# Kernel tuning notes

Measured on AMD Instinct MI355X. Metric: run time of the kernel, lower is better.

The kernel has to match this reference:

```python
import jax, jax.numpy as jnp
import numpy as np

HIDDEN = 256   # HIDDEN_NUM
INPUT = 4      # fixed input_size
B, T = 128, 512


def _lstm_dir(xs, wi, wh, bi, bh):
    """Single-direction LSTM scan. xs: [T,B,D]; wi: [4H,D]; wh: [4H,H]; bi,bh: [4H].
    PyTorch gate order: i, f, g, o. Returns hidden states [T,B,H]."""
    Tn, Bn, _ = xs.shape
    Hn = wh.shape[1]
    # precompute input contribution for all timesteps (tiny D -> one big GEMM)
    gx = jnp.einsum('tbd,gd->tbg', xs, wi) + bi + bh  # [T,B,4H]

    def step(carry, g):
        h, c = carry
        g = g + h @ wh.T
        i, f, gg, o = jnp.split(g, 4, axis=-1)
        c = jax.nn.sigmoid(f) * c + jax.nn.sigmoid(i) * jnp.tanh(gg)
        h = jax.nn.sigmoid(o) * jnp.tanh(c)
        return (h, c), h

    init = (jnp.zeros((Bn, Hn), xs.dtype), jnp.zeros((Bn, Hn), xs.dtype))
    _, hs = jax.lax.scan(step, init, gx)
    return hs


def _lstm_bidir(xs, w_ih, w_hh, b_ih, b_hh):
    """xs: [T,B,D]; weights stacked over direction: w_ih [2,4H,D] etc. -> [T,B,2H]."""
    fwd = _lstm_dir(xs, w_ih[0], w_hh[0], b_ih[0], b_hh[0])
    bwd = _lstm_dir(xs[::-1], w_ih[1], w_hh[1], b_ih[1], b_hh[1])[::-1]
    return jnp.concatenate([fwd, bwd], axis=-1)


def setup_inputs() -> dict:
    key = jax.random.key(0)
    ks = jax.random.split(key, 12)
    k = 1.0 / np.sqrt(HIDDEN)
    u = lambda kk, shape: jax.random.uniform(kk, shape, jnp.float32, -k, k)
    H4 = 4 * HIDDEN
    return {
        'x': jax.random.normal(ks[0], (B, T, INPUT), jnp.float32),
        # layer 0 (input size 4), stacked [fwd, bwd]
        'w_ih0': u(ks[1], (2, H4, INPUT)),
        'w_hh0': u(ks[2], (2, H4, HIDDEN)),
        'b_ih0': u(ks[3], (2, H4)),
        'b_hh0': u(ks[4], (2, H4)),
        # layer 1 (input size 2H from bidirectional layer 0)
        'w_ih1': u(ks[5], (2, H4, 2 * HIDDEN)),
        'w_hh1': u(ks[6], (2, H4, HIDDEN)),
        'b_ih1': u(ks[7], (2, H4)),
        'b_hh1': u(ks[8], (2, H4)),
        # final linear: HIDDEN*2 -> 2
        'fc_w': u(ks[9], (2, 2 * HIDDEN)),
        'fc_b': u(ks[10], (2,)),
    }


def reference(x, w_ih0, w_hh0, b_ih0, b_hh0, w_ih1, w_hh1, b_ih1, b_hh1, fc_w, fc_b):
    xs = jnp.transpose(x, (1, 0, 2))                 # [T,B,4] (seq-major like torch)
    h0 = _lstm_bidir(xs, w_ih0, w_hh0, b_ih0, b_hh0)  # [T,B,2H]
    h1 = _lstm_bidir(h0, w_ih1, w_hh1, b_ih1, b_hh1)  # [T,B,2H]
    pooled = jnp.mean(h1, axis=0)                     # [B,2H]
    return pooled @ fc_w.T + fc_b                     # [B,2]
```

## Files before the change

kernel.cpp:

```cpp
#include <hip/hip_runtime.h>
#include <hip/hip_bf16.h>


typedef __bf16 bf16;
typedef __bf16 bf16x8 __attribute__((ext_vector_type(8)));
typedef float  f32x4  __attribute__((ext_vector_type(4)));
typedef unsigned int u32;
typedef unsigned long long u64;
typedef u64 u64x2 __attribute__((ext_vector_type(2)));

#define T_SEQ 512
#define BATCH 128
#define HID   256

#define H0_BYTES   67239936ULL
#define H1_BYTES   262144ULL
#define POOL_BYTES 262144ULL
#define FL0_OFF    (H0_BYTES + H1_BYTES + POOL_BYTES)
#define FL1_OFF    (FL0_OFF + 4096ULL)

#define MFMA16(a, b, c) __builtin_amdgcn_mfma_f32_16x16x32_bf16((a), (b), (c), 0, 0, 0)
#define AL(p)     __hip_atomic_load((p), __ATOMIC_RELAXED, __HIP_MEMORY_SCOPE_AGENT)
#define AS(p, v)  __hip_atomic_store((p), (v), __ATOMIC_RELAXED, __HIP_MEMORY_SCOPE_AGENT)

__device__ __forceinline__ float fsig(float v) {
    return __builtin_amdgcn_rcpf(1.0f + __expf(-v));
}
__device__ __forceinline__ float ftanh(float v) {
    float a = fabsf(v);
    float e = __expf(-2.0f * a);
    float r = (1.0f - e) * __builtin_amdgcn_rcpf(1.0f + e);
    return v < 0.0f ? -r : r;
}

__global__ void k_init(unsigned int* ws_u, int* flags0, int* flags1) {
    const int t = blockIdx.x * 256 + threadIdx.x;
    ws_u[t] = 0u;
    ws_u[(size_t)513 * 16384 + t] = 0u;
    unsigned int* h1u = ws_u + (H0_BYTES / 4);
    h1u[t] = 0u;
    h1u[32768 + t] = 0u;
    if (t < 1024) flags0[t] = 0;
    if (t < 2048) flags1[t] = 0;
}

__global__ __launch_bounds__(256, 1) void k_l0(
    const float* __restrict__ x, const float* __restrict__ wih,
    const float* __restrict__ whh, const float* __restrict__ bih,
    const float* __restrict__ bhh, bf16* __restrict__ h0,
    int* __restrict__ flags)
{
    __shared__ __align__(16) bf16 Hs[64][20];

    const int blk = blockIdx.x;
    const int dir = blk >> 5, bh = (blk >> 4) & 1, g = blk & 15;
    const int tid = threadIdx.x, wave = tid >> 6, lane = tid & 63;
    const int l15 = lane & 15, q = lane >> 4;
    const int j = g * 16 + l15;

    bf16x8 Bf[4][8];
#pragma unroll
    for (int tg = 0; tg < 4; ++tg) {
        const float* wr = whh + ((size_t)(dir * 1024 + tg * 256 + j)) * 256 + q * 8;
#pragma unroll
        for (int kt = 0; kt < 8; ++kt) {
            f32x4 aa = *(const f32x4*)(wr + kt * 32);
            f32x4 bb = *(const f32x4*)(wr + kt * 32 + 4);
            bf16x8 f;
            f[0] = (bf16)aa[0]; f[1] = (bf16)aa[1]; f[2] = (bf16)aa[2]; f[3] = (bf16)aa[3];
            f[4] = (bf16)bb[0]; f[5] = (bf16)bb[1]; f[6] = (bf16)bb[2]; f[7] = (bf16)bb[3];
            Bf[tg][kt] = f;
        }
    }
    float biasg[4], wx[4][4];
#pragma unroll
    for (int tg = 0; tg < 4; ++tg) {
        const int n = dir * 1024 + tg * 256 + j;
        biasg[tg] = bih[n] + bhh[n];
#pragma unroll
        for (int d2 = 0; d2 < 4; ++d2) wx[tg][d2] = wih[(size_t)n * 4 + d2];
    }

    float c4[4] = {0.f, 0.f, 0.f, 0.f};
    const int arow  = bh * 64 + wave * 16 + l15;
    const int lrow0 = wave * 16 + q * 4;
    const int mrow0 = bh * 64 + lrow0;
    const int srow = tid >> 2, scg = (tid & 3) * 4;
    int* fgrp = flags + (dir * 2 + bh) * 256;
    int budget = 30000000;

#pragma unroll 1
    for (int s = 1; s <= T_SEQ; ++s) {
        const int t_in = dir ? (T_SEQ - s) : (s - 1);

        f32x4 xv[4];
#pragma unroll
        for (int r = 0; r < 4; ++r)
            xv[r] = *(const f32x4*)(x + ((size_t)(mrow0 + r) * T_SEQ + t_in) * 4);
        f32x4 acc[4];
#pragma unroll
        for (int tg = 0; tg < 4; ++tg) {
#pragma unroll
            for (int r = 0; r < 4; ++r) {
                acc[tg][r] = biasg[tg] + xv[r][0] * wx[tg][0] + xv[r][1] * wx[tg][1]
                                       + xv[r][2] * wx[tg][2] + xv[r][3] * wx[tg][3];
            }
        }

        if (lane < 16) {
            const int need = s - 1;
            while (AL(fgrp + lane * 16) < need) {
                if (--budget < 0) break;
            }
        }
        asm volatile("" ::: "memory");

        const u64* hsrc = (const u64*)(h0 + ((size_t)(dir * 513 + (s - 1)) * BATCH + arow) * HID)
                          + q * 2;
        u64 av[16];
#pragma unroll
        for (int kt = 0; kt < 8; ++kt) {
            av[2 * kt]     = AL(hsrc + kt * 8);
            av[2 * kt + 1] = AL(hsrc + kt * 8 + 1);
        }
#pragma unroll
        for (int kt = 0; kt < 8; ++kt) {
            u64x2 t2; t2[0] = av[2 * kt]; t2[1] = av[2 * kt + 1];
            const bf16x8 A = __builtin_bit_cast(bf16x8, t2);
            acc[0] = MFMA16(A, Bf[0][kt], acc[0]);
            acc[1] = MFMA16(A, Bf[1][kt], acc[1]);
            acc[2] = MFMA16(A, Bf[2][kt], acc[2]);
            acc[3] = MFMA16(A, Bf[3][kt], acc[3]);
        }

#pragma unroll
        for (int r = 0; r < 4; ++r) {
            const float iv = fsig(acc[0][r]);
            const float fv = fsig(acc[1][r]);
            const float gv = ftanh(acc[2][r]);
            const float ov = fsig(acc[3][r]);
            c4[r] = fv * c4[r] + iv * gv;
            const float hv = ov * ftanh(c4[r]);
            Hs[lrow0 + r][l15] = (bf16)hv;
        }
        __syncthreads();
        {
            const u64 hv8 = *(const u64*)&Hs[srow][scg];
            u64* dst = (u64*)(h0 + ((size_t)(dir * 513 + s) * BATCH + bh * 64 + srow) * HID
                              + g * 16 + scg);
            AS(dst, hv8);
        }
        __syncthreads();
        if (tid == 0) AS(fgrp + g * 16, s);
    }
}

__global__ __launch_bounds__(256, 1) void k_l1(
    const float* __restrict__ wih1, const float* __restrict__ whh1,
    const float* __restrict__ bih1, const float* __restrict__ bhh1,
    bf16* __restrict__ h0, bf16* __restrict__ h1,
    float* __restrict__ pooled, int* __restrict__ flags)
{
    __shared__ float Gs[4][32][17];
    __shared__ __align__(16) bf16 Hs[32][20];
    __shared__ __align__(16) bf16 As1[32][264];

    const int blk = blockIdx.x;
    const int dir = blk >> 6, bq = (blk >> 4) & 3, g = blk & 15;
    const int tid = threadIdx.x, wave = tid >> 6, lane = tid & 63;
    const int l15 = lane & 15, q = lane >> 4;
    const int n = dir * 1024 + wave * 256 + g * 16 + l15;

    bf16x8 Bf[24];
#pragma unroll
    for (int kt = 0; kt < 24; ++kt) {
        const int k = kt * 32 + q * 8;
        const float* src = (kt < 8) ? (whh1 + (size_t)n * 256 + k)
                                    : (wih1 + (size_t)n * 512 + (k - 256));
        f32x4 aa = *(const f32x4*)src;
        f32x4 bb = *(const f32x4*)(src + 4);
        bf16x8 f;
        f[0] = (bf16)aa[0]; f[1] = (bf16)aa[1]; f[2] = (bf16)aa[2]; f[3] = (bf16)aa[3];
        f[4] = (bf16)bb[0]; f[5] = (bf16)bb[1]; f[6] = (bf16)bb[2]; f[7] = (bf16)bb[3];
        Bf[kt] = f;
    }
    const float biasw = bih1[n] + bhh1[n];
    const int r0 = tid >> 4, colu = tid & 15;
    float cst[2] = {0.f, 0.f}, pool[2] = {0.f, 0.f};
    int* fgrp = flags + (dir * 4 + bq) * 256;
    int budget = 30000000;

#pragma unroll 1
    for (int s = 1; s <= T_SEQ; ++s) {
        const int slotf = dir ? (513 - s) : s;
        const int slotb = dir ? s : (513 - s);

        f32x4 acc0 = {biasw, biasw, biasw, biasw};
        f32x4 acc1 = acc0;
        const bf16* f0 = h0 + ((size_t)slotf * BATCH + bq * 32 + l15) * HID + q * 8;
        const bf16* b0 = h0 + ((size_t)(513 + slotb) * BATCH + bq * 32 + l15) * HID + q * 8;
#pragma unroll
        for (int kt = 0; kt < 8; ++kt) {
            const bf16x8 af0 = *(const bf16x8*)(f0 + kt * 32);
            const bf16x8 af1 = *(const bf16x8*)(f0 + 16 * HID + kt * 32);
            acc0 = MFMA16(af0, Bf[8 + kt], acc0);
            acc1 = MFMA16(af1, Bf[8 + kt], acc1);
        }
#pragma unroll
        for (int kt = 0; kt < 8; ++kt) {
            const bf16x8 ab0 = *(const bf16x8*)(b0 + kt * 32);
            const bf16x8 ab1 = *(const bf16x8*)(b0 + 16 * HID + kt * 32);
            acc0 = MFMA16(ab0, Bf[16 + kt], acc0);
            acc1 = MFMA16(ab1, Bf[16 + kt], acc1);
        }

        if (lane < 16) {
            const int need = s - 1;
            while (AL(fgrp + lane * 16) < need) {
                if (--budget < 0) break;
            }
        }
        asm volatile("" ::: "memory");

        {
            const u64* hb = (const u64*)(h1 + ((size_t)(dir * 2 + ((s - 1) & 1)) * BATCH
                                               + bq * 32) * HID);
#pragma unroll
            for (int i = 0; i < 4; ++i) {
                const int chunk = tid + 256 * i;
                const int row = chunk >> 5, cc = chunk & 31;
                const u64 lo = AL(hb + (size_t)row * 64 + cc * 2);
                const u64 hi = AL(hb + (size_t)row * 64 + cc * 2 + 1);
                u64x2 t2; t2[0] = lo; t2[1] = hi;
                *(bf16x8*)(&As1[row][cc * 8]) = __builtin_bit_cast(bf16x8, t2);
            }
        }
        __syncthreads();

#pragma unroll
        for (int kt = 0; kt < 8; ++kt) {
            const bf16x8 a0 = *(const bf16x8*)(&As1[l15][kt * 32 + q * 8]);
            const bf16x8 a1 = *(const bf16x8*)(&As1[16 + l15][kt * 32 + q * 8]);
            acc0 = MFMA16(a0, Bf[kt], acc0);
            acc1 = MFMA16(a1, Bf[kt], acc1);
        }

#pragma unroll
        for (int r = 0; r < 4; ++r) {
            Gs[wave][q * 4 + r][l15]      = acc0[r];
            Gs[wave][16 + q * 4 + r][l15] = acc1[r];
        }
        __syncthreads();

#pragma unroll
        for (int rr = 0; rr < 2; ++rr) {
            const int r = r0 + rr * 16;
            const float iv = fsig(Gs[0][r][colu]);
            const float fv = fsig(Gs[1][r][colu]);
            const float gv = ftanh(Gs[2][r][colu]);
            const float ov = fsig(Gs[3][r][colu]);
            cst[rr] = fv * cst[rr] + iv * gv;
            const float hv = ov * ftanh(cst[rr]);
            pool[rr] += hv;
            Hs[r][colu] = (bf16)hv;
        }
        __syncthreads();
        {
            const int lrow = tid >> 3, c2 = (tid & 7) * 2;
            const u32 hv4 = *(const u32*)&Hs[lrow][c2];
            u32* dst = (u32*)(h1 + ((size_t)(dir * 2 + (s & 1)) * BATCH + bq * 32 + lrow) * HID
                              + g * 16 + c2);
            AS(dst, hv4);
        }
        __syncthreads();
        if (tid == 0) AS(fgrp + g * 16, s);
    }
#pragma unroll
    for (int rr = 0; rr < 2; ++rr) {
        const int r = r0 + rr * 16;
        pooled[((size_t)dir * BATCH + bq * 32 + r) * HID + g * 16 + colu] =
            pool[rr] * (1.0f / 512.0f);
    }
}

__global__ void k_fc(const float* __restrict__ pooled, const float* __restrict__ fcw,
                     const float* __restrict__ fcb, float* __restrict__ out)
{
    const int b = blockIdx.x;
    const int lane = threadIdx.x;
    float s0 = 0.f, s1 = 0.f;
#pragma unroll
    for (int jj = 0; jj < 8; ++jj) {
        const int jx = lane + jj * 64;
        const float p = (jx < 256) ? pooled[(size_t)b * 256 + jx]
                                   : pooled[32768 + (size_t)b * 256 + (jx - 256)];
        s0 += p * fcw[jx];
        s1 += p * fcw[512 + jx];
    }
#pragma unroll
    for (int off = 32; off > 0; off >>= 1) {
        s0 += __shfl_down(s0, off);
        s1 += __shfl_down(s1, off);
    }
    if (lane == 0) {
        out[b * 2 + 0] = s0 + fcb[0];
        out[b * 2 + 1] = s1 + fcb[1];
    }
}

extern "C" void kernel_launch(void* const* d_in, const int* in_sizes, int n_in,
                              void* d_out, int out_size, void* d_ws, size_t ws_size,
                              hipStream_t stream)
{
    const float* x    = (const float*)d_in[0];
    const float* wih0 = (const float*)d_in[1];
    const float* whh0 = (const float*)d_in[2];
    const float* bih0 = (const float*)d_in[3];
    const float* bhh0 = (const float*)d_in[4];
    const float* wih1 = (const float*)d_in[5];
    const float* whh1 = (const float*)d_in[6];
    const float* bih1 = (const float*)d_in[7];
    const float* bhh1 = (const float*)d_in[8];
    const float* fcw  = (const float*)d_in[9];
    const float* fcb  = (const float*)d_in[10];
    float* out = (float*)d_out;

    char* ws = (char*)d_ws;
    bf16* h0      = (bf16*)ws;
    bf16* h1      = (bf16*)(ws + H0_BYTES);
    float* pooled = (float*)(ws + H0_BYTES + H1_BYTES);
    int* flags0   = (int*)(ws + FL0_OFF);
    int* flags1   = (int*)(ws + FL1_OFF);

    k_init<<<dim3(64), dim3(256), 0, stream>>>((unsigned int*)ws, flags0, flags1);
    k_l0<<<dim3(64), dim3(256), 0, stream>>>(x, wih0, whh0, bih0, bhh0, h0, flags0);
    k_l1<<<dim3(128), dim3(256), 0, stream>>>(wih1, whh1, bih1, bhh1, h0, h1, pooled, flags1);
    k_fc<<<dim3(128), dim3(64), 0, stream>>>(pooled, fcw, fcb, out);
}
```

Measured before the change: 4.864 ms.

## Interleave both LSTM directions in each block to hide cross-block sync latency

Each block of the layer-0 and layer-1 recurrent kernels now handles both directions, alternating forward and backward steps, so half as many blocks are launched. A direction's flag is published before its h-store, to signal readiness earlier, and the wait on one direction overlaps the other direction's compute. Layer 1 also stages its layer-0 inputs through LDS, loading them before the spin-wait. This doubles register use for weights (48 bf16x8 in layer 1) and shifts the flag protocol, which risks spills, reduced parallelism, and ordering hazards from publishing early.

New measurement: 6.594 ms. 1.36x slower.

```diff
diff --git a/kernel.cpp b/kernel.cpp
--- a/kernel.cpp
+++ b/kernel.cpp
@@ -50,108 +50,113 @@
     const float* __restrict__ bhh, bf16* __restrict__ h0,
     int* __restrict__ flags)
 {
-    __shared__ __align__(16) bf16 Hs[64][20];
+    __shared__ __align__(16) bf16 Hs[2][64][20];
 
     const int blk = blockIdx.x;
-    const int dir = blk >> 5, bh = (blk >> 4) & 1, g = blk & 15;
+    const int bh = blk >> 4, g = blk & 15;
     const int tid = threadIdx.x, wave = tid >> 6, lane = tid & 63;
     const int l15 = lane & 15, q = lane >> 4;
     const int j = g * 16 + l15;
 
-    bf16x8 Bf[4][8];
-#pragma unroll
-    for (int tg = 0; tg < 4; ++tg) {
-        const float* wr = whh + ((size_t)(dir * 1024 + tg * 256 + j)) * 256 + q * 8;
-#pragma unroll
-        for (int kt = 0; kt < 8; ++kt) {
-            f32x4 aa = *(const f32x4*)(wr + kt * 32);
-            f32x4 bb = *(const f32x4*)(wr + kt * 32 + 4);
-            bf16x8 f;
-            f[0] = (bf16)aa[0]; f[1] = (bf16)aa[1]; f[2] = (bf16)aa[2]; f[3] = (bf16)aa[3];
-            f[4] = (bf16)bb[0]; f[5] = (bf16)bb[1]; f[6] = (bf16)bb[2]; f[7] = (bf16)bb[3];
-            Bf[tg][kt] = f;
-        }
-    }
-    float biasg[4], wx[4][4];
-#pragma unroll
-    for (int tg = 0; tg < 4; ++tg) {
-        const int n = dir * 1024 + tg * 256 + j;
-        biasg[tg] = bih[n] + bhh[n];
-#pragma unroll
-        for (int d2 = 0; d2 < 4; ++d2) wx[tg][d2] = wih[(size_t)n * 4 + d2];
-    }
-
-    float c4[4] = {0.f, 0.f, 0.f, 0.f};
+    bf16x8 Bf[2][4][8];
+    float biasg[2][4], wx[2][4][4];
+#pragma unroll
+    for (int dir = 0; dir < 2; ++dir) {
+#pragma unroll
+        for (int tg = 0; tg < 4; ++tg) {
+            const float* wr = whh + ((size_t)(dir * 1024 + tg * 256 + j)) * 256 + q * 8;
+#pragma unroll
+            for (int kt = 0; kt < 8; ++kt) {
+                f32x4 aa = *(const f32x4*)(wr + kt * 32);
+                f32x4 bb = *(const f32x4*)(wr + kt * 32 + 4);
+                bf16x8 f;
+                f[0] = (bf16)aa[0]; f[1] = (bf16)aa[1]; f[2] = (bf16)aa[2]; f[3] = (bf16)aa[3];
+                f[4] = (bf16)bb[0]; f[5] = (bf16)bb[1]; f[6] = (bf16)bb[2]; f[7] = (bf16)bb[3];
+                Bf[dir][tg][kt] = f;
+            }
+            const int n = dir * 1024 + tg * 256 + j;
+            biasg[dir][tg] = bih[n] + bhh[n];
+#pragma unroll
+            for (int d2 = 0; d2 < 4; ++d2) wx[dir][tg][d2] = wih[(size_t)n * 4 + d2];
+        }
+    }
+
+    float c4[2][4] = {{0.f, 0.f, 0.f, 0.f}, {0.f, 0.f, 0.f, 0.f}};
     const int arow  = bh * 64 + wave * 16 + l15;
     const int lrow0 = wave * 16 + q * 4;
     const int mrow0 = bh * 64 + lrow0;
     const int srow = tid >> 2, scg = (tid & 3) * 4;
-    int* fgrp = flags + (dir * 2 + bh) * 256;
+    int* fg0 = flags + (0 * 2 + bh) * 256;
+    int* fg1 = flags + (1 * 2 + bh) * 256;
     int budget = 30000000;
 
 #pragma unroll 1
     for (int s = 1; s <= T_SEQ; ++s) {
-        const int t_in = dir ? (T_SEQ - s) : (s - 1);
-
-        f32x4 xv[4];
-#pragma unroll
-        for (int r = 0; r < 4; ++r)
-            xv[r] = *(const f32x4*)(x + ((size_t)(mrow0 + r) * T_SEQ + t_in) * 4);
-        f32x4 acc[4];
-#pragma unroll
-        for (int tg = 0; tg < 4; ++tg) {
+#pragma unroll
+        for (int dir = 0; dir < 2; ++dir) {
+            int* fgrp = dir ? fg1 : fg0;
+            const int t_in = dir ? (T_SEQ - s) : (s - 1);
+
+            f32x4 xv[4];
+#pragma unroll
+            for (int r = 0; r < 4; ++r)
+                xv[r] = *(const f32x4*)(x + ((size_t)(mrow0 + r) * T_SEQ + t_in) * 4);
+            f32x4 acc[4];
+#pragma unroll
+            for (int tg = 0; tg < 4; ++tg) {
+#pragma unroll
+                for (int r = 0; r < 4; ++r) {
+                    acc[tg][r] = biasg[dir][tg]
+                               + xv[r][0] * wx[dir][tg][0] + xv[r][1] * wx[dir][tg][1]
+                               + xv[r][2] * wx[dir][tg][2] + xv[r][3] * wx[dir][tg][3];
+                }
+            }
+
+            if (lane < 16) {
+                const int need = s - 1;
+                while (AL(fgrp + lane * 16) < need) {
+                    if (--budget < 0) break;
+                }
+            }
+            asm volatile("" ::: "memory");
+
+            const u64* hsrc = (const u64*)(h0 + ((size_t)(dir * 513 + (s - 1)) * BATCH + arow) * HID)
+                              + q * 2;
+            u64 av[16];
+#pragma unroll
+            for (int kt = 0; kt < 8; ++kt) {
+                av[2 * kt]     = AL(hsrc + kt * 8);
+                av[2 * kt + 1] = AL(hsrc + kt * 8 + 1);
+            }
+#pragma unroll
+            for (int kt = 0; kt < 8; ++kt) {
+                u64x2 t2; t2[0] = av[2 * kt]; t2[1] = av[2 * kt + 1];
+                const bf16x8 A = __builtin_bit_cast(bf16x8, t2);
+                acc[0] = MFMA16(A, Bf[dir][0][kt], acc[0]);
+                acc[1] = MFMA16(A, Bf[dir][1][kt], acc[1]);
+                acc[2] = MFMA16(A, Bf[dir][2][kt], acc[2]);
+                acc[3] = MFMA16(A, Bf[dir][3][kt], acc[3]);
+            }
+
 #pragma unroll
             for (int r = 0; r < 4; ++r) {
-                acc[tg][r] = biasg[tg] + xv[r][0] * wx[tg][0] + xv[r][1] * wx[tg][1]
-                                       + xv[r][2] * wx[tg][2] + xv[r][3] * wx[tg][3];
-            }
-        }
-
-        if (lane < 16) {
-            const int need = s - 1;
-            while (AL(fgrp + lane * 16) < need) {
-                if (--budget < 0) break;
-            }
-        }
-        asm volatile("" ::: "memory");
-
-        const u64* hsrc = (const u64*)(h0 + ((size_t)(dir * 513 + (s - 1)) * BATCH + arow) * HID)
-                          + q * 2;
-        u64 av[16];
-#pragma unroll
-        for (int kt = 0; kt < 8; ++kt) {
-            av[2 * kt]     = AL(hsrc + kt * 8);
-            av[2 * kt + 1] = AL(hsrc + kt * 8 + 1);
-        }
-#pragma unroll
-        for (int kt = 0; kt < 8; ++kt) {
-            u64x2 t2; t2[0] = av[2 * kt]; t2[1] = av[2 * kt + 1];
-            const bf16x8 A = __builtin_bit_cast(bf16x8, t2);
-            acc[0] = MFMA16(A, Bf[0][kt], acc[0]);
-            acc[1] = MFMA16(A, Bf[1][kt], acc[1]);
-            acc[2] = MFMA16(A, Bf[2][kt], acc[2]);
-            acc[3] = MFMA16(A, Bf[3][kt], acc[3]);
-        }
-
-#pragma unroll
-        for (int r = 0; r < 4; ++r) {
-            const float iv = fsig(acc[0][r]);
-            const float fv = fsig(acc[1][r]);
-            const float gv = ftanh(acc[2][r]);
-            const float ov = fsig(acc[3][r]);
-            c4[r] = fv * c4[r] + iv * gv;
-            const float hv = ov * ftanh(c4[r]);
-            Hs[lrow0 + r][l15] = (bf16)hv;
-        }
-        __syncthreads();
-        {
-            const u64 hv8 = *(const u64*)&Hs[srow][scg];
-            u64* dst = (u64*)(h0 + ((size_t)(dir * 513 + s) * BATCH + bh * 64 + srow) * HID
-                              + g * 16 + scg);
-            AS(dst, hv8);
-        }
-        __syncthreads();
-        if (tid == 0) AS(fgrp + g * 16, s);
+                const float iv = fsig(acc[0][r]);
+                const float fv = fsig(acc[1][r]);
+                const float gv = ftanh(acc[2][r]);
+                const float ov = fsig(acc[3][r]);
+                c4[dir][r] = fv * c4[dir][r] + iv * gv;
+                const float hv = ov * ftanh(c4[dir][r]);
+                Hs[dir][lrow0 + r][l15] = (bf16)hv;
+            }
+            __syncthreads();
+            if (tid == 0) AS((dir ? fg0 : fg1) + g * 16, dir ? s : (s - 1));
+            {
+                const u64 hv8 = *(const u64*)&Hs[dir][srow][scg];
+                u64* dst = (u64*)(h0 + ((size_t)(dir * 513 + s) * BATCH + bh * 64 + srow) * HID
+                                  + g * 16 + scg);
+                AS(dst, hv8);
+            }
+        }
     }
 }
 
@@ -164,122 +169,154 @@
     __shared__ float Gs[4][32][17];
     __shared__ __align__(16) bf16 Hs[32][20];
     __shared__ __align__(16) bf16 As1[32][264];
+    __shared__ __align__(16) bf16 Ah0[32][520];
 
     const int blk = blockIdx.x;
-    const int dir = blk >> 6, bq = (blk >> 4) & 3, g = blk & 15;
+    const int bq = blk >> 4, g = blk & 15;
     const int tid = threadIdx.x, wave = tid >> 6, lane = tid & 63;
     const int l15 = lane & 15, q = lane >> 4;
-    const int n = dir * 1024 + wave * 256 + g * 16 + l15;
-
-    bf16x8 Bf[24];
-#pragma unroll
-    for (int kt = 0; kt < 24; ++kt) {
-        const int k = kt * 32 + q * 8;
-        const float* src = (kt < 8) ? (whh1 + (size_t)n * 256 + k)
-                                    : (wih1 + (size_t)n * 512 + (k - 256));
-        f32x4 aa = *(const f32x4*)src;
-        f32x4 bb = *(const f32x4*)(src + 4);
-        bf16x8 f;
-        f[0] = (bf16)aa[0]; f[1] = (bf16)aa[1]; f[2] = (bf16)aa[2]; f[3] = (bf16)aa[3];
-        f[4] = (bf16)bb[0]; f[5] = (bf16)bb[1]; f[6] = (bf16)bb[2]; f[7] = (bf16)bb[3];
-        Bf[kt] = f;
-    }
-    const float biasw = bih1[n] + bhh1[n];
+
+    bf16x8 Bf[2][24];
+    float biasw[2];
+#pragma unroll
+    for (int dir = 0; dir < 2; ++dir) {
+        const int n = dir * 1024 + wave * 256 + g * 16 + l15;
+#pragma unroll
+        for (int kt = 0; kt < 24; ++kt) {
+            const int k = kt * 32 + q * 8;
+            const float* src = (kt < 8) ? (whh1 + (size_t)n * 256 + k)
+                                        : (wih1 + (size_t)n * 512 + (k - 256));
+            f32x4 aa = *(const f32x4*)src;
+            f32x4 bb = *(const f32x4*)(src + 4);
+            bf16x8 f;
+            f[0] = (bf16)aa[0]; f[1] = (bf16)aa[1]; f[2] = (bf16)aa[2]; f[3] = (bf16)aa[3];
+            f[4] = (bf16)bb[0]; f[5] = (bf16)bb[1]; f[6] = (bf16)bb[2]; f[7] = (bf16)bb[3];
+            Bf[dir][kt] = f;
+        }
+        biasw[dir] = bih1[n] + bhh1[n];
+    }
     const int r0 = tid >> 4, colu = tid & 15;
-    float cst[2] = {0.f, 0.f}, pool[2] = {0.f, 0.f};
-    int* fgrp = flags + (dir * 4 + bq) * 256;
+    float cst[2][2] = {{0.f, 0.f}, {0.f, 0.f}};
+    float pool[2][2] = {{0.f, 0.f}, {0.f, 0.f}};
+    int* fg0 = flags + (0 * 4 + bq) * 256;
+    int* fg1 = flags + (1 * 4 + bq) * 256;
     int budget = 30000000;
 
 #pragma unroll 1
     for (int s = 1; s <= T_SEQ; ++s) {
-        const int slotf = dir ? (513 - s) : s;
-        const int slotb = dir ? s : (513 - s);
-
-        f32x4 acc0 = {biasw, biasw, biasw, biasw};
-        f32x4 acc1 = acc0;
-        const bf16* f0 = h0 + ((size_t)slotf * BATCH + bq * 32 + l15) * HID + q * 8;
-        const bf16* b0 = h0 + ((size_t)(513 + slotb) * BATCH + bq * 32 + l15) * HID + q * 8;
-#pragma unroll
-        for (int kt = 0; kt < 8; ++kt) {
-            const bf16x8 af0 = *(const bf16x8*)(f0 + kt * 32);
-            const bf16x8 af1 = *(const bf16x8*)(f0 + 16 * HID + kt * 32);
-            acc0 = MFMA16(af0, Bf[8 + kt], acc0);
-            acc1 = MFMA16(af1, Bf[8 + kt], acc1);
-        }
-#pragma unroll
-        for (int kt = 0; kt < 8; ++kt) {
-            const bf16x8 ab0 = *(const bf16x8*)(b0 + kt * 32);
-            const bf16x8 ab1 = *(const bf16x8*)(b0 + 16 * HID + kt * 32);
-            acc0 = MFMA16(ab0, Bf[16 + kt], acc0);
-            acc1 = MFMA16(ab1, Bf[16 + kt], acc1);
-        }
-
-        if (lane < 16) {
-            const int need = s - 1;
-            while (AL(fgrp + lane * 16) < need) {
-                if (--budget < 0) break;
-            }
-        }
-        asm volatile("" ::: "memory");
-
-        {
+#pragma unroll
+        for (int dir = 0; dir < 2; ++dir) {
+            int* fgrp = dir ? fg1 : fg0;
+            const int slotf = dir ? (513 - s) : s;
+            const int slotb = dir ? s : (513 - s);
+
+            bf16x8 hstage[8];
+#pragma unroll
+            for (int i = 0; i < 8; ++i) {
+                const int chunk = tid + 256 * i;
+                const int row = chunk >> 6, cc = chunk & 63;
+                const bf16* src = (cc < 32)
+                    ? h0 + ((size_t)slotf * BATCH + bq * 32 + row) * HID + cc * 8
+                    : h0 + ((size_t)(513 + slotb) * BATCH + bq * 32 + row) * HID + (cc - 32) * 8;
+                hstage[i] = *(const bf16x8*)src;
+            }
+
+            if (lane < 16) {
+                const int need = s - 1;
+                while (AL(fgrp + lane * 16) < need) {
+                    if (--budget < 0) break;
+                }
+            }
+            asm volatile("" ::: "memory");
+
+            u64 alo[4], ahi[4];
             const u64* hb = (const u64*)(h1 + ((size_t)(dir * 2 + ((s - 1) & 1)) * BATCH
                                                + bq * 32) * HID);
 #pragma unroll
             for (int i = 0; i < 4; ++i) {
                 const int chunk = tid + 256 * i;
                 const int row = chunk >> 5, cc = chunk & 31;
-                const u64 lo = AL(hb + (size_t)row * 64 + cc * 2);
-                const u64 hi = AL(hb + (size_t)row * 64 + cc * 2 + 1);
-                u64x2 t2; t2[0] = lo; t2[1] = hi;
+                alo[i] = AL(hb + (size_t)row * 64 + cc * 2);
+                ahi[i] = AL(hb + (size_t)row * 64 + cc * 2 + 1);
+            }
+
+#pragma unroll
+            for (int i = 0; i < 8; ++i) {
+                const int chunk = tid + 256 * i;
+                const int row = chunk >> 6, cc = chunk & 63;
+                *(bf16x8*)(&Ah0[row][cc * 8]) = hstage[i];
+            }
+#pragma unroll
+            for (int i = 0; i < 4; ++i) {
+                const int chunk = tid + 256 * i;
+                const int row = chunk >> 5, cc = chunk & 31;
+                u64x2 t2; t2[0] = alo[i]; t2[1] = ahi[i];
                 *(bf16x8*)(&As1[row][cc * 8]) = __builtin_bit_cast(bf16x8, t2);
             }
-        }
-        __syncthreads();
-
-#pragma unroll
-        for (int kt = 0; kt < 8; ++kt) {
-            const bf16x8 a0 = *(const bf16x8*)(&As1[l15][kt * 32 + q * 8]);
-            const bf16x8 a1 = *(const bf16x8*)(&As1[16 + l15][kt * 32 + q * 8]);
-            acc0 = MFMA16(a0, Bf[kt], acc0);
-            acc1 = MFMA16(a1, Bf[kt], acc1);
-        }
-
-#pragma unroll
-        for (int r = 0; r < 4; ++r) {
-            Gs[wave][q * 4 + r][l15]      = acc0[r];
-            Gs[wave][16 + q * 4 + r][l15] = acc1[r];
-        }
-        __syncthreads();
-
+            __syncthreads();
+            if (tid == 0) AS((dir ? fg0 : fg1) + g * 16, dir ? s : (s - 1));
+
+            f32x4 acc0 = {biasw[dir], biasw[dir], biasw[dir], biasw[dir]};
+            f32x4 acc1 = acc0;
+#pragma unroll
+            for (int kt = 0; kt < 8; ++kt) {
+                const bf16x8 a0 = *(const bf16x8*)(&Ah0[l15][kt * 32 + q * 8]);
+                const bf16x8 a1 = *(const bf16x8*)(&Ah0[16 + l15][kt * 32 + q * 8]);
+                acc0 = MFMA16(a0, Bf[dir][8 + kt], acc0);
+                acc1 = MFMA16(a1, Bf[dir][8 + kt], acc1);
+            }
+#pragma unroll
+            for (int kt = 0; kt < 8; ++kt) {
+                const bf16x8 a0 = *(const bf16x8*)(&Ah0[l15][256 + kt * 32 + q * 8]);
+                const bf16x8 a1 = *(const bf16x8*)(&Ah0[16 + l15][256 + kt * 32 + q * 8]);
+                acc0 = MFMA16(a0, Bf[dir][16 + kt], acc0);
+                acc1 = MFMA16(a1, Bf[dir][16 + kt], acc1);
+            }
+#pragma unroll
+            for (int kt = 0; kt < 8; ++kt) {
+                const bf16x8 a0 = *(const bf16x8*)(&As1[l15][kt * 32 + q * 8]);
+                const bf16x8 a1 = *(const bf16x8*)(&As1[16 + l15][kt * 32 + q * 8]);
+                acc0 = MFMA16(a0, Bf[dir][kt], acc0);
+                acc1 = MFMA16(a1, Bf[dir][kt], acc1);
+            }
+
+#pragma unroll
+            for (int r = 0; r < 4; ++r) {
+                Gs[wave][q * 4 + r][l15]      = acc0[r];
+                Gs[wave][16 + q * 4 + r][l15] = acc1[r];
+            }
+            __syncthreads();
+
+#pragma unroll
+            for (int rr = 0; rr < 2; ++rr) {
+                const int r = r0 + rr * 16;
+                const float iv = fsig(Gs[0][r][colu]);
+                const float fv = fsig(Gs[1][r][colu]);
+                const float gv = ftanh(Gs[2][r][colu]);
+                const float ov = fsig(Gs[3][r][colu]);
+                cst[dir][rr] = fv * cst[dir][rr] + iv * gv;
+                const float hv = ov * ftanh(cst[dir][rr]);
+                pool[dir][rr] += hv;
+                Hs[r][colu] = (bf16)hv;
+            }
+            __syncthreads();
+            {
+                const int lrow = tid >> 3, c2 = (tid & 7) * 2;
+                const u32 hv4 = *(const u32*)&Hs[lrow][c2];
+                u32* dst = (u32*)(h1 + ((size_t)(dir * 2 + (s & 1)) * BATCH + bq * 32 + lrow) * HID
+                                  + g * 16 + c2);
+                AS(dst, hv4);
+            }
+        }
+    }
+#pragma unroll
+    for (int dir = 0; dir < 2; ++dir) {
 #pragma unroll
         for (int rr = 0; rr < 2; ++rr) {
             const int r = r0 + rr * 16;
-            const float iv = fsig(Gs[0][r][colu]);
-            const float fv = fsig(Gs[1][r][colu]);
-            const float gv = ftanh(Gs[2][r][colu]);
-            const float ov = fsig(Gs[3][r][colu]);
-            cst[rr] = fv * cst[rr] + iv * gv;
-            const float hv = ov * ftanh(cst[rr]);
-            pool[rr] += hv;
-            Hs[r][colu] = (bf16)hv;
-        }
-        __syncthreads();
-        {
-            const int lrow = tid >> 3, c2 = (tid & 7) * 2;
-            const u32 hv4 = *(const u32*)&Hs[lrow][c2];
-            u32* dst = (u32*)(h1 + ((size_t)(dir * 2 + (s & 1)) * BATCH + bq * 32 + lrow) * HID
-                              + g * 16 + c2);
-            AS(dst, hv4);
-        }
-        __syncthreads();
-        if (tid == 0) AS(fgrp + g * 16, s);
-    }
-#pragma unroll
-    for (int rr = 0; rr < 2; ++rr) {
-        const int r = r0 + rr * 16;
-        pooled[((size_t)dir * BATCH + bq * 32 + r) * HID + g * 16 + colu] =
-            pool[rr] * (1.0f / 512.0f);
+            pooled[((size_t)dir * BATCH + bq * 32 + r) * HID + g * 16 + colu] =
+                pool[dir][rr] * (1.0f / 512.0f);
+        }
     }
 }
 
@@ -333,7 +370,7 @@
     int* flags1   = (int*)(ws + FL1_OFF);
 
     k_init<<<dim3(64), dim3(256), 0, stream>>>((unsigned int*)ws, flags0, flags1);
-    k_l0<<<dim3(64), dim3(256), 0, stream>>>(x, wih0, whh0, bih0, bhh0, h0, flags0);
-    k_l1<<<dim3(128), dim3(256), 0, stream>>>(wih1, whh1, bih1, bhh1, h0, h1, pooled, flags1);
+    k_l0<<<dim3(32), dim3(256), 0, stream>>>(x, wih0, whh0, bih0, bhh0, h0, flags0);
+    k_l1<<<dim3(64), dim3(256), 0, stream>>>(wih1, whh1, bih1, bhh1, h0, h1, pooled, flags1);
     k_fc<<<dim3(128), dim3(64), 0, stream>>>(pooled, fcw, fcb, out);
 }
```

## Replace layer-0 flag synchronization with NaN-canary polling on hidden-state buffer

Applied to the files above, without the earlier changes.

Layer 0 no longer waits on per-group progress flags before reading the previous timestep's hidden state. Instead the init kernel fills the whole h0 buffer with a bf16 NaN canary, and each wave re-reads its h slice until no canary value remains. The LDS staging buffer is double-buffered so the second barrier and the flag store can be dropped. This takes a flag round trip and a barrier off the serial recurrence, at the cost of a full 67MB canary fill in init. It also relies on 64-bit atomic stores being seen whole, and on a real h value never equalling the canary.

After: 4.887 ms. About the same (+0.5%).

```diff
diff --git a/kernel.cpp b/kernel.cpp
--- a/kernel.cpp
+++ b/kernel.cpp
@@ -19,6 +19,9 @@
 #define FL0_OFF    (H0_BYTES + H1_BYTES + POOL_BYTES)
 #define FL1_OFF    (FL0_OFF + 4096ULL)
 
+#define CANARY16 0x7FC0u
+#define CANARY32 0x7FC07FC0u
+
 #define MFMA16(a, b, c) __builtin_amdgcn_mfma_f32_16x16x32_bf16((a), (b), (c), 0, 0, 0)
 #define AL(p)     __hip_atomic_load((p), __ATOMIC_RELAXED, __HIP_MEMORY_SCOPE_AGENT)
 #define AS(p, v)  __hip_atomic_store((p), (v), __ATOMIC_RELAXED, __HIP_MEMORY_SCOPE_AGENT)
@@ -33,24 +36,29 @@
     return v < 0.0f ? -r : r;
 }
 
-__global__ void k_init(unsigned int* ws_u, int* flags0, int* flags1) {
-    const int t = blockIdx.x * 256 + threadIdx.x;
-    ws_u[t] = 0u;
-    ws_u[(size_t)513 * 16384 + t] = 0u;
-    unsigned int* h1u = ws_u + (H0_BYTES / 4);
-    h1u[t] = 0u;
-    h1u[32768 + t] = 0u;
-    if (t < 1024) flags0[t] = 0;
-    if (t < 2048) flags1[t] = 0;
+__global__ void k_init(u32* h0u, u32* h1u, int* flags0, int* flags1) {
+    const u32 gt = blockIdx.x * 256 + threadIdx.x;
+    const u32 N = 2u * 513u * 16384u;
+    const u32 stride = gridDim.x * 256;
+    for (u32 i = gt; i < N; i += stride) {
+        const u32 sg = i >> 14;
+        const u32 v = (sg == 0u || sg == 513u) ? 0u : CANARY32;
+        h0u[i] = v;
+    }
+    if (gt < 16384) {
+        h1u[gt] = 0u;
+        h1u[32768 + gt] = 0u;
+    }
+    if (gt < 1024) flags0[gt] = 0;
+    if (gt < 2048) flags1[gt] = 0;
 }
 
 __global__ __launch_bounds__(256, 1) void k_l0(
     const float* __restrict__ x, const float* __restrict__ wih,
     const float* __restrict__ whh, const float* __restrict__ bih,
-    const float* __restrict__ bhh, bf16* __restrict__ h0,
-    int* __restrict__ flags)
+    const float* __restrict__ bhh, bf16* __restrict__ h0)
 {
-    __shared__ __align__(16) bf16 Hs[64][20];
+    __shared__ __align__(16) bf16 Hs[2][64][20];
 
     const int blk = blockIdx.x;
     const int dir = blk >> 5, bh = (blk >> 4) & 1, g = blk & 15;
@@ -86,7 +94,6 @@
     const int lrow0 = wave * 16 + q * 4;
     const int mrow0 = bh * 64 + lrow0;
     const int srow = tid >> 2, scg = (tid & 3) * 4;
-    int* fgrp = flags + (dir * 2 + bh) * 256;
     int budget = 30000000;
 
 #pragma unroll 1
@@ -107,22 +114,22 @@
             }
         }
 
-        if (lane < 16) {
-            const int need = s - 1;
-            while (AL(fgrp + lane * 16) < need) {
-                if (--budget < 0) break;
-            }
-        }
-        asm volatile("" ::: "memory");
-
         const u64* hsrc = (const u64*)(h0 + ((size_t)(dir * 513 + (s - 1)) * BATCH + arow) * HID)
                           + q * 2;
         u64 av[16];
-#pragma unroll
-        for (int kt = 0; kt < 8; ++kt) {
-            av[2 * kt]     = AL(hsrc + kt * 8);
-            av[2 * kt + 1] = AL(hsrc + kt * 8 + 1);
-        }
+        while (true) {
+#pragma unroll
+            for (int kt = 0; kt < 8; ++kt) {
+                av[2 * kt]     = AL(hsrc + kt * 8);
+                av[2 * kt + 1] = AL(hsrc + kt * 8 + 1);
+            }
+            u32 bad = 0u;
+#pragma unroll
+            for (int i = 0; i < 16; ++i)
+                bad |= (((u32)av[i] & 0xFFFFu) == CANARY16) ? 1u : 0u;
+            if (!__any(bad) || --budget < 0) break;
+        }
+
 #pragma unroll
         for (int kt = 0; kt < 8; ++kt) {
             u64x2 t2; t2[0] = av[2 * kt]; t2[1] = av[2 * kt + 1];
@@ -133,6 +140,7 @@
             acc[3] = MFMA16(A, Bf[3][kt], acc[3]);
         }
 
+        const int par = s & 1;
 #pragma unroll
         for (int r = 0; r < 4; ++r) {
             const float iv = fsig(acc[0][r]);
@@ -141,17 +149,15 @@
             const float ov = fsig(acc[3][r]);
             c4[r] = fv * c4[r] + iv * gv;
             const float hv = ov * ftanh(c4[r]);
-            Hs[lrow0 + r][l15] = (bf16)hv;
+            Hs[par][lrow0 + r][l15] = (bf16)hv;
         }
         __syncthreads();
         {
-            const u64 hv8 = *(const u64*)&Hs[srow][scg];
+            const u64 hv8 = *(const u64*)&Hs[par][srow][scg];
             u64* dst = (u64*)(h0 + ((size_t)(dir * 513 + s) * BATCH + bh * 64 + srow) * HID
                               + g * 16 + scg);
             AS(dst, hv8);
         }
-        __syncthreads();
-        if (tid == 0) AS(fgrp + g * 16, s);
     }
 }
 
@@ -332,8 +338,9 @@
     int* flags0   = (int*)(ws + FL0_OFF);
     int* flags1   = (int*)(ws + FL1_OFF);
 
-    k_init<<<dim3(64), dim3(256), 0, stream>>>((unsigned int*)ws, flags0, flags1);
-    k_l0<<<dim3(64), dim3(256), 0, stream>>>(x, wih0, whh0, bih0, bhh0, h0, flags0);
+    k_init<<<dim3(2048), dim3(256), 0, stream>>>((u32*)ws, (u32*)(ws + H0_BYTES),
+                                                 flags0, flags1);
+    k_l0<<<dim3(64), dim3(256), 0, stream>>>(x, wih0, whh0, bih0, bhh0, h0);
     k_l1<<<dim3(128), dim3(256), 0, stream>>>(wih1, whh1, bih1, bhh1, h0, h1, pooled, flags1);
     k_fc<<<dim3(128), dim3(64), 0, stream>>>(pooled, fcw, fcb, out);
 }
```

## Consolidate LSTM recurrence into fewer, larger blocks to cut cross-block sync

Applied to the files above, without the earlier changes.

Both recurrent kernels now use 512-thread blocks that each own more hidden units and batch rows. Layer 0 goes from 64 to 16 blocks and layer 1 from 128 to 32, so each timestep spin-waits on fewer flags (4 or 8 instead of 16). The intent is to shorten the per-step global flag handshake latency that dominates a serial scan. The cost is fewer CUs doing the work, with each block running more MFMA and gate work per step, and higher register and LDS pressure.

After: 14.22 ms. +192.4%, slower.

```diff
diff --git a/kernel.cpp b/kernel.cpp
--- a/kernel.cpp
+++ b/kernel.cpp
@@ -44,24 +44,27 @@
     if (t < 2048) flags1[t] = 0;
 }
 
-__global__ __launch_bounds__(256, 1) void k_l0(
+__global__ __launch_bounds__(512, 2) void k_l0(
     const float* __restrict__ x, const float* __restrict__ wih,
     const float* __restrict__ whh, const float* __restrict__ bih,
     const float* __restrict__ bhh, bf16* __restrict__ h0,
     int* __restrict__ flags)
 {
-    __shared__ __align__(16) bf16 Hs[64][20];
+    __shared__ __align__(16) bf16 Hs[64][72];
 
     const int blk = blockIdx.x;
-    const int dir = blk >> 5, bh = (blk >> 4) & 1, g = blk & 15;
+    const int dir = blk >> 3, bh = (blk >> 2) & 1, g = blk & 3;
     const int tid = threadIdx.x, wave = tid >> 6, lane = tid & 63;
     const int l15 = lane & 15, q = lane >> 4;
-    const int j = g * 16 + l15;
+    const int ug = wave & 3, mh = wave >> 2;
+    const int j = g * 64 + ug * 16 + l15;
 
     bf16x8 Bf[4][8];
+    float biasg[4], wx[4][4];
 #pragma unroll
     for (int tg = 0; tg < 4; ++tg) {
-        const float* wr = whh + ((size_t)(dir * 1024 + tg * 256 + j)) * 256 + q * 8;
+        const int n = dir * 1024 + tg * 256 + j;
+        const float* wr = whh + (size_t)n * 256 + q * 8;
 #pragma unroll
         for (int kt = 0; kt < 8; ++kt) {
             f32x4 aa = *(const f32x4*)(wr + kt * 32);
@@ -71,43 +74,38 @@
             f[4] = (bf16)bb[0]; f[5] = (bf16)bb[1]; f[6] = (bf16)bb[2]; f[7] = (bf16)bb[3];
             Bf[tg][kt] = f;
         }
-    }
-    float biasg[4], wx[4][4];
-#pragma unroll
-    for (int tg = 0; tg < 4; ++tg) {
-        const int n = dir * 1024 + tg * 256 + j;
         biasg[tg] = bih[n] + bhh[n];
 #pragma unroll
-        for (int d2 = 0; d2 < 4; ++d2) wx[tg][d2] = wih[(size_t)n * 4 + d2];
-    }
-
-    float c4[4] = {0.f, 0.f, 0.f, 0.f};
-    const int arow  = bh * 64 + wave * 16 + l15;
-    const int lrow0 = wave * 16 + q * 4;
-    const int mrow0 = bh * 64 + lrow0;
-    const int srow = tid >> 2, scg = (tid & 3) * 4;
-    int* fgrp = flags + (dir * 2 + bh) * 256;
+        for (int d = 0; d < 4; ++d) wx[tg][d] = wih[(size_t)n * 4 + d];
+    }
+
+    float c4[2][4] = {};
+    const int rbase = bh * 64 + mh * 32;
+    int* fgrp = flags + (dir * 2 + bh) * 64;
     int budget = 30000000;
 
 #pragma unroll 1
     for (int s = 1; s <= T_SEQ; ++s) {
         const int t_in = dir ? (T_SEQ - s) : (s - 1);
 
-        f32x4 xv[4];
-#pragma unroll
-        for (int r = 0; r < 4; ++r)
-            xv[r] = *(const f32x4*)(x + ((size_t)(mrow0 + r) * T_SEQ + t_in) * 4);
-        f32x4 acc[4];
-#pragma unroll
-        for (int tg = 0; tg < 4; ++tg) {
-#pragma unroll
-            for (int r = 0; r < 4; ++r) {
-                acc[tg][r] = biasg[tg] + xv[r][0] * wx[tg][0] + xv[r][1] * wx[tg][1]
-                                       + xv[r][2] * wx[tg][2] + xv[r][3] * wx[tg][3];
-            }
-        }
-
-        if (lane < 16) {
+        f32x4 acc[4][2];
+#pragma unroll
+        for (int Mt = 0; Mt < 2; ++Mt) {
+            f32x4 xv[4];
+#pragma unroll
+            for (int r = 0; r < 4; ++r)
+                xv[r] = *(const f32x4*)(x + ((size_t)(rbase + Mt * 16 + q * 4 + r) * T_SEQ
+                                             + t_in) * 4);
+#pragma unroll
+            for (int tg = 0; tg < 4; ++tg)
+#pragma unroll
+                for (int r = 0; r < 4; ++r)
+                    acc[tg][Mt][r] = biasg[tg]
+                        + xv[r][0] * wx[tg][0] + xv[r][1] * wx[tg][1]
+                        + xv[r][2] * wx[tg][2] + xv[r][3] * wx[tg][3];
+        }
+
+        if (lane < 4) {
             const int need = s - 1;
             while (AL(fgrp + lane * 16) < need) {
                 if (--budget < 0) break;
@@ -115,61 +113,69 @@
         }
         asm volatile("" ::: "memory");
 
-        const u64* hsrc = (const u64*)(h0 + ((size_t)(dir * 513 + (s - 1)) * BATCH + arow) * HID)
-                          + q * 2;
-        u64 av[16];
-#pragma unroll
-        for (int kt = 0; kt < 8; ++kt) {
-            av[2 * kt]     = AL(hsrc + kt * 8);
-            av[2 * kt + 1] = AL(hsrc + kt * 8 + 1);
-        }
-#pragma unroll
-        for (int kt = 0; kt < 8; ++kt) {
-            u64x2 t2; t2[0] = av[2 * kt]; t2[1] = av[2 * kt + 1];
-            const bf16x8 A = __builtin_bit_cast(bf16x8, t2);
-            acc[0] = MFMA16(A, Bf[0][kt], acc[0]);
-            acc[1] = MFMA16(A, Bf[1][kt], acc[1]);
-            acc[2] = MFMA16(A, Bf[2][kt], acc[2]);
-            acc[3] = MFMA16(A, Bf[3][kt], acc[3]);
-        }
-
-#pragma unroll
-        for (int r = 0; r < 4; ++r) {
-            const float iv = fsig(acc[0][r]);
-            const float fv = fsig(acc[1][r]);
-            const float gv = ftanh(acc[2][r]);
-            const float ov = fsig(acc[3][r]);
-            c4[r] = fv * c4[r] + iv * gv;
-            const float hv = ov * ftanh(c4[r]);
-            Hs[lrow0 + r][l15] = (bf16)hv;
-        }
-        __syncthreads();
+#pragma unroll
+        for (int Mt = 0; Mt < 2; ++Mt) {
+            const u64* hsrc = (const u64*)(h0 + ((size_t)(dir * 513 + (s - 1)) * BATCH
+                                                 + rbase + Mt * 16 + l15) * HID) + q * 2;
+            u64 av[16];
+#pragma unroll
+            for (int kt = 0; kt < 8; ++kt) {
+                av[2 * kt]     = AL(hsrc + kt * 8);
+                av[2 * kt + 1] = AL(hsrc + kt * 8 + 1);
+            }
+#pragma unroll
+            for (int kt = 0; kt < 8; ++kt) {
+                u64x2 t2; t2[0] = av[2 * kt]; t2[1] = av[2 * kt + 1];
+                const bf16x8 A = __builtin_bit_cast(bf16x8, t2);
+                acc[0][Mt] = MFMA16(A, Bf[0][kt], acc[0][Mt]);
+                acc[1][Mt] = MFMA16(A, Bf[1][kt], acc[1][Mt]);
+                acc[2][Mt] = MFMA16(A, Bf[2][kt], acc[2][Mt]);
+                acc[3][Mt] = MFMA16(A, Bf[3][kt], acc[3][Mt]);
+            }
+        }
+
+#pragma unroll
+        for (int Mt = 0; Mt < 2; ++Mt)
+#pragma unroll
+            for (int r = 0; r < 4; ++r) {
+                const float iv = fsig(acc[0][Mt][r]);
+                const float fv = fsig(acc[1][Mt][r]);
+                const float gv = ftanh(acc[2][Mt][r]);
+                const float ov = fsig(acc[3][Mt][r]);
+                c4[Mt][r] = fv * c4[Mt][r] + iv * gv;
+                const float hv = ov * ftanh(c4[Mt][r]);
+                Hs[mh * 32 + Mt * 16 + q * 4 + r][ug * 16 + l15] = (bf16)hv;
+            }
+        __syncthreads();
+
         {
-            const u64 hv8 = *(const u64*)&Hs[srow][scg];
-            u64* dst = (u64*)(h0 + ((size_t)(dir * 513 + s) * BATCH + bh * 64 + srow) * HID
-                              + g * 16 + scg);
-            AS(dst, hv8);
+            const int row = tid >> 3, u0 = (tid & 7) * 8;
+            u64* dst = (u64*)(h0 + ((size_t)(dir * 513 + s) * BATCH + bh * 64 + row) * HID
+                              + g * 64 + u0);
+            AS(dst,     *(const u64*)&Hs[row][u0]);
+            AS(dst + 1, *(const u64*)&Hs[row][u0 + 4]);
         }
         __syncthreads();
         if (tid == 0) AS(fgrp + g * 16, s);
     }
 }
 
-__global__ __launch_bounds__(256, 1) void k_l1(
+__global__ __launch_bounds__(512, 2) void k_l1(
     const float* __restrict__ wih1, const float* __restrict__ whh1,
     const float* __restrict__ bih1, const float* __restrict__ bhh1,
     bf16* __restrict__ h0, bf16* __restrict__ h1,
     float* __restrict__ pooled, int* __restrict__ flags)
 {
-    __shared__ float Gs[4][32][17];
-    __shared__ __align__(16) bf16 Hs[32][20];
-    __shared__ __align__(16) bf16 As1[32][264];
+    __shared__ float Gs[4][64][33];
+    __shared__ __align__(16) bf16 Hs[64][40];
+    __shared__ __align__(16) bf16 As1[64][264];
 
     const int blk = blockIdx.x;
-    const int dir = blk >> 6, bq = (blk >> 4) & 3, g = blk & 15;
+    const int dir = blk >> 4, bq = (blk >> 3) & 1, g = blk & 7;
     const int tid = threadIdx.x, wave = tid >> 6, lane = tid & 63;
     const int l15 = lane & 15, q = lane >> 4;
-    const int n = dir * 1024 + wave * 256 + g * 16 + l15;
+    const int gate = wave & 3, uh = wave >> 2;
+    const int n = dir * 1024 + gate * 256 + g * 32 + uh * 16 + l15;
 
     bf16x8 Bf[24];
 #pragma unroll
@@ -185,9 +191,9 @@
         Bf[kt] = f;
     }
     const float biasw = bih1[n] + bhh1[n];
-    const int r0 = tid >> 4, colu = tid & 15;
-    float cst[2] = {0.f, 0.f}, pool[2] = {0.f, 0.f};
-    int* fgrp = flags + (dir * 4 + bq) * 256;
+    const int r0 = tid >> 5, colu = tid & 31;
+    float cst[4] = {}, pool[4] = {};
+    int* fgrp = flags + (dir * 2 + bq) * 128;
     int budget = 30000000;
 
 #pragma unroll 1
@@ -195,26 +201,32 @@
         const int slotf = dir ? (513 - s) : s;
         const int slotb = dir ? s : (513 - s);
 
-        f32x4 acc0 = {biasw, biasw, biasw, biasw};
-        f32x4 acc1 = acc0;
-        const bf16* f0 = h0 + ((size_t)slotf * BATCH + bq * 32 + l15) * HID + q * 8;
-        const bf16* b0 = h0 + ((size_t)(513 + slotb) * BATCH + bq * 32 + l15) * HID + q * 8;
+        f32x4 acc[4];
+#pragma unroll
+        for (int Mt = 0; Mt < 4; ++Mt) {
+            acc[Mt][0] = biasw; acc[Mt][1] = biasw;
+            acc[Mt][2] = biasw; acc[Mt][3] = biasw;
+        }
+        const bf16* f0 = h0 + ((size_t)slotf * BATCH + bq * 64 + l15) * HID + q * 8;
+        const bf16* b0 = h0 + ((size_t)(513 + slotb) * BATCH + bq * 64 + l15) * HID + q * 8;
 #pragma unroll
         for (int kt = 0; kt < 8; ++kt) {
-            const bf16x8 af0 = *(const bf16x8*)(f0 + kt * 32);
-            const bf16x8 af1 = *(const bf16x8*)(f0 + 16 * HID + kt * 32);
-            acc0 = MFMA16(af0, Bf[8 + kt], acc0);
-            acc1 = MFMA16(af1, Bf[8 + kt], acc1);
+#pragma unroll
+            for (int Mt = 0; Mt < 4; ++Mt) {
+                const bf16x8 af = *(const bf16x8*)(f0 + (size_t)Mt * 16 * HID + kt * 32);
+                acc[Mt] = MFMA16(af, Bf[8 + kt], acc[Mt]);
+            }
         }
 #pragma unroll
         for (int kt = 0; kt < 8; ++kt) {
-            const bf16x8 ab0 = *(const bf16x8*)(b0 + kt * 32);
-            const bf16x8 ab1 = *(const bf16x8*)(b0 + 16 * HID + kt * 32);
-            acc0 = MFMA16(ab0, Bf[16 + kt], acc0);
-            acc1 = MFMA16(ab1, Bf[16 + kt], acc1);
-        }
-
-        if (lane < 16) {
+#pragma unroll
+            for (int Mt = 0; Mt < 4; ++Mt) {
+                const bf16x8 ab = *(const bf16x8*)(b0 + (size_t)Mt * 16 * HID + kt * 32);
+                acc[Mt] = MFMA16(ab, Bf[16 + kt], acc[Mt]);
+            }
+        }
+
+        if (lane < 8) {
             const int need = s - 1;
             while (AL(fgrp + lane * 16) < need) {
                 if (--budget < 0) break;
@@ -224,10 +236,10 @@
 
         {
             const u64* hb = (const u64*)(h1 + ((size_t)(dir * 2 + ((s - 1) & 1)) * BATCH
-                                               + bq * 32) * HID);
+                                               + bq * 64) * HID);
 #pragma unroll
             for (int i = 0; i < 4; ++i) {
-                const int chunk = tid + 256 * i;
+                const int chunk = tid + 512 * i;
                 const int row = chunk >> 5, cc = chunk & 31;
                 const u64 lo = AL(hb + (size_t)row * 64 + cc * 2);
                 const u64 hi = AL(hb + (size_t)row * 64 + cc * 2 + 1);
@@ -239,21 +251,22 @@
 
 #pragma unroll
         for (int kt = 0; kt < 8; ++kt) {
-            const bf16x8 a0 = *(const bf16x8*)(&As1[l15][kt * 32 + q * 8]);
-            const bf16x8 a1 = *(const bf16x8*)(&As1[16 + l15][kt * 32 + q * 8]);
-            acc0 = MFMA16(a0, Bf[kt], acc0);
-            acc1 = MFMA16(a1, Bf[kt], acc1);
-        }
-
-#pragma unroll
-        for (int r = 0; r < 4; ++r) {
-            Gs[wave][q * 4 + r][l15]      = acc0[r];
-            Gs[wave][16 + q * 4 + r][l15] = acc1[r];
-        }
-        __syncthreads();
-
-#pragma unroll
-        for (int rr = 0; rr < 2; ++rr) {
+#pragma unroll
+            for (int Mt = 0; Mt < 4; ++Mt) {
+                const bf16x8 a = *(const bf16x8*)(&As1[Mt * 16 + l15][kt * 32 + q * 8]);
+                acc[Mt] = MFMA16(a, Bf[kt], acc[Mt]);
+            }
+        }
+
+#pragma unroll
+        for (int Mt = 0; Mt < 4; ++Mt)
+#pragma unroll
+            for (int r = 0; r < 4; ++r)
+                Gs[gate][Mt * 16 + q * 4 + r][uh * 16 + l15] = acc[Mt][r];
+        __syncthreads();
+
+#pragma unroll
+        for (int rr = 0; rr < 4; ++rr) {
             const int r = r0 + rr * 16;
             const float iv = fsig(Gs[0][r][colu]);
             const float fv = fsig(Gs[1][r][colu]);
@@ -265,20 +278,21 @@
             Hs[r][colu] = (bf16)hv;
         }
         __syncthreads();
+
         {
-            const int lrow = tid >> 3, c2 = (tid & 7) * 2;
-            const u32 hv4 = *(const u32*)&Hs[lrow][c2];
-            u32* dst = (u32*)(h1 + ((size_t)(dir * 2 + (s & 1)) * BATCH + bq * 32 + lrow) * HID
-                              + g * 16 + c2);
-            AS(dst, hv4);
+            const int row = tid >> 3, c4u = (tid & 7) * 4;
+            u64* dst = (u64*)(h1 + ((size_t)(dir * 2 + (s & 1)) * BATCH + bq * 64 + row) * HID
+                              + g * 32 + c4u);
+            AS(dst, *(const u64*)&Hs[row][c4u]);
         }
         __syncthreads();
         if (tid == 0) AS(fgrp + g * 16, s);
     }
-#pragma unroll
-    for (int rr = 0; rr < 2; ++rr) {
-        const int r = r0 + rr * 16;
-        pooled[((size_t)dir * BATCH + bq * 32 + r) * HID + g * 16 + colu] =
+
+#pragma unroll
+    for (int rr = 0; rr < 4; ++rr) {
+        const int row = r0 + rr * 16;
+        pooled[((size_t)dir * BATCH + bq * 64 + row) * HID + g * 32 + colu] =
             pool[rr] * (1.0f / 512.0f);
     }
 }
@@ -333,7 +347,7 @@
     int* flags1   = (int*)(ws + FL1_OFF);
 
     k_init<<<dim3(64), dim3(256), 0, stream>>>((unsigned int*)ws, flags0, flags1);
-    k_l0<<<dim3(64), dim3(256), 0, stream>>>(x, wih0, whh0, bih0, bhh0, h0, flags0);
-    k_l1<<<dim3(128), dim3(256), 0, stream>>>(wih1, whh1, bih1, bhh1, h0, h1, pooled, flags1);
+    k_l0<<<dim3(16), dim3(512), 0, stream>>>(x, wih0, whh0, bih0, bhh0, h0, flags0);
+    k_l1<<<dim3(32), dim3(512), 0, stream>>>(wih1, whh1, bih1, bhh1, h0, h1, pooled, flags1);
     k_fc<<<dim3(128), dim3(64), 0, stream>>>(pooled, fcw, fcb, out);
 }
```
